# Optimization experiments

Hardware: AMD Instinct MI355X
Metric: run time of the kernel (lower is better)

The kernel has to match this reference:

```python
import jax, jax.numpy as jnp
import numpy as np

B, I, H, O = 16384, 512, 1024, 512

def setup_inputs() -> dict:
    key = jax.random.key(0)
    ks = jax.random.split(key, 8)
    s_x = 1.0 / np.sqrt(I)
    s_h = 1.0 / np.sqrt(H)
    inp = jax.random.normal(ks[0], (B, I), jnp.float32)
    h = jax.random.normal(ks[1], (B, H), jnp.float32)
    c = jax.random.normal(ks[2], (B, H), jnp.float32)
    # stacked gate weights, order [i, o, f, z]
    Wx = jax.random.uniform(ks[3], (4, H, I), jnp.float32, -s_x, s_x)
    Wh = jax.random.uniform(ks[4], (4, H, H), jnp.float32, -s_h, s_h)
    # z-gate h2z weight is re-initialized with standard normal in reset_parameters
    Wh = Wh.at[3].set(jax.random.normal(ks[5], (H, H), jnp.float32))
    # biases per module init: i=linspace(-1,-10), o=0, f=linspace(1,10), z=0
    bx = jnp.stack([
        jnp.linspace(-1.0, -10.0, H, dtype=jnp.float32),
        jnp.zeros((H,), jnp.float32),
        jnp.linspace(1.0, 10.0, H, dtype=jnp.float32),
        jnp.zeros((H,), jnp.float32),
    ])
    Wout = jax.random.uniform(ks[6], (O, H), jnp.float32, -s_h, s_h)
    bout = jax.random.uniform(ks[7], (O,), jnp.float32, -s_h, s_h)
    return {"inp": inp, "h": h, "c": c, "Wx": Wx, "bx": bx, "Wh": Wh,
            "Wout": Wout, "bout": bout}

def reference(inp, h, c, Wx, bx, Wh, Wout, bout):
    # fused gate pre-activations: two stacked GEMMs
    # gx: [4, B, H], gh: [4, B, H]
    gx = jnp.einsum('bi,ghi->gbh', inp, Wx) + bx[:, None, :]
    gh = jnp.einsum('bh,gkh->gbk', h, Wh)
    g = gx + gh
    i = jax.nn.sigmoid(g[0])
    o = jax.nn.sigmoid(g[1])
    f = jax.nn.sigmoid(g[2])
    z = jnp.tanh(g[3])
    c_new = i * z + f * c
    h_new = o * jnp.tanh(c_new)  # act_fn = tanh
    out = h_new @ Wout.T + bout
    return (out, h_new)
```

## Files before the change

kernel.cpp:

```cpp
#include <hip/hip_runtime.h>
#include <stdint.h>

#define BB 16384
#define II 512
#define HH 1024
#define OO 512

typedef short s16x8 __attribute__((ext_vector_type(8)));
typedef float f32x4 __attribute__((ext_vector_type(4)));

__device__ __forceinline__ unsigned short f2bf(float x) {
  union { float f; unsigned u; } v; v.f = x;
  return (unsigned short)((v.u + 0x7fffu + ((v.u >> 16) & 1u)) >> 16);
}
__device__ __forceinline__ float bf2f(unsigned short b) {
  union { unsigned u; float f; } v; v.u = ((unsigned)b) << 16;
  return v.f;
}
__device__ __forceinline__ float sigmoid_f(float x) {
  return 1.0f / (1.0f + __expf(-x));
}
__device__ __forceinline__ float tanh_f(float x) {
  float ax = fabsf(x);
  float e = __expf(-2.0f * ax);
  float t = (1.0f - e) / (1.0f + e);
  return x >= 0.0f ? t : -t;
}

__device__ __forceinline__ void stage16(const void* g, void* l) {
  __builtin_amdgcn_global_load_lds((const __attribute__((address_space(1))) void*)g,
                                   (__attribute__((address_space(3))) void*)l,
                                   16, 0, 0);
}

__device__ __forceinline__ void mma_step64(const unsigned short* As, const unsigned short* Bs,
                                           f32x4 acc[4][4], int lane, int wave) {
  const int wm = wave & 1, wn = wave >> 1;
  const int ln = lane & 15, q = lane >> 4;
#pragma unroll
  for (int s = 0; s < 2; ++s) {
    s16x8 af[4], bfr[4];
#pragma unroll
    for (int i = 0; i < 4; ++i) {
      const int r = wm * 64 + i * 16 + ln;
      af[i] = *(const s16x8*)(As + r * 64 + ((((s << 2) + q) + r) & 7) * 8);
    }
#pragma unroll
    for (int i = 0; i < 4; ++i) {
      const int r = wn * 64 + i * 16 + ln;
      bfr[i] = *(const s16x8*)(Bs + r * 64 + ((((s << 2) + q) + r) & 7) * 8);
    }
#pragma unroll
    for (int mi = 0; mi < 4; ++mi)
#pragma unroll
      for (int ni = 0; ni < 4; ++ni)
        acc[mi][ni] = __builtin_amdgcn_mfma_f32_16x16x32_bf16(af[mi], bfr[ni], acc[mi][ni], 0, 0, 0);
  }
}


__global__ __launch_bounds__(256) void prep_X(const float* __restrict__ inp,
                                              const float* __restrict__ h,
                                              unsigned short* __restrict__ Xb,
                                              unsigned short* __restrict__ Hlo) {
  int t = blockIdx.x * 256 + threadIdx.x;
  int base = t * 8;
  int b = base / 1536;
  int k = base - b * 1536;
  const float* src = (k < 512) ? (inp + b * 512 + k) : (h + b * 1024 + (k - 512));
  float4 v0 = *(const float4*)src;
  float4 v1 = *(const float4*)(src + 4);
  float f[8] = {v0.x, v0.y, v0.z, v0.w, v1.x, v1.y, v1.z, v1.w};
  unsigned short hi[8];
#pragma unroll
  for (int i = 0; i < 8; ++i) hi[i] = f2bf(f[i]);
  *(s16x8*)(Xb + base) = *(s16x8*)hi;
  if (k >= 512) {
    unsigned short lo[8];
#pragma unroll
    for (int i = 0; i < 8; ++i) lo[i] = f2bf(f[i] - bf2f(hi[i]));
    *(s16x8*)(Hlo + b * 1024 + (k - 512)) = *(s16x8*)lo;
  }
}

__global__ __launch_bounds__(256) void prep_Wg(const float* __restrict__ Wx,
                                               const float* __restrict__ Wh,
                                               unsigned short* __restrict__ Wg) {
  int t = blockIdx.x * 256 + threadIdx.x;
  int base = t * 8;
  int n = base / 1536;
  int k = base - n * 1536;
  int r = n & 255;
  int gate = (r >> 4) & 3;
  int unit = ((n >> 8) << 6) + (((r >> 6) & 3) << 4) + (r & 15);
  const float* src = (k < 512) ? (Wx + (gate * 1024 + unit) * 512 + k)
                               : (Wh + (gate * 1024 + unit) * 1024 + (k - 512));
  float4 v0 = *(const float4*)src;
  float4 v1 = *(const float4*)(src + 4);
  float f[8] = {v0.x, v0.y, v0.z, v0.w, v1.x, v1.y, v1.z, v1.w};
  unsigned short o[8];
#pragma unroll
  for (int i = 0; i < 8; ++i) o[i] = f2bf(f[i]);
  *(s16x8*)(Wg + base) = *(s16x8*)o;
}

__global__ __launch_bounds__(256) void prep_Wz2(const float* __restrict__ Whz,
                                                unsigned short* __restrict__ Wz2) {
  int t = blockIdx.x * 256 + threadIdx.x;
  int base = t * 8;
  int n = base >> 11;
  int k = base & 2047;
  int klo = (k < 1024) ? k : (k - 1024);
  const float* src = Whz + n * 1024 + klo;
  float4 v0 = *(const float4*)src;
  float4 v1 = *(const float4*)(src + 4);
  float f[8] = {v0.x, v0.y, v0.z, v0.w, v1.x, v1.y, v1.z, v1.w};
  unsigned short o[8];
  if (k < 1024) {
#pragma unroll
    for (int i = 0; i < 8; ++i) { unsigned short h_ = f2bf(f[i]); o[i] = f2bf(f[i] - bf2f(h_)); }
  } else {
#pragma unroll
    for (int i = 0; i < 8; ++i) o[i] = f2bf(f[i]);
  }
  *(s16x8*)(Wz2 + base) = *(s16x8*)o;
}

__global__ __launch_bounds__(256) void prep_Wout(const float* __restrict__ Wout,
                                                 unsigned short* __restrict__ Wo) {
  int t = blockIdx.x * 256 + threadIdx.x;
  int base = t * 8;
  float4 v0 = *(const float4*)(Wout + base);
  float4 v1 = *(const float4*)(Wout + base + 4);
  float f[8] = {v0.x, v0.y, v0.z, v0.w, v1.x, v1.y, v1.z, v1.w};
  unsigned short o[8];
#pragma unroll
  for (int i = 0; i < 8; ++i) o[i] = f2bf(f[i]);
  *(s16x8*)(Wo + base) = *(s16x8*)o;
}


#define RD_A(CA, MI, KS) (*(const s16x8*)((CA) + ((KS) ? aoff1 : aoff0) + (MI) * 1024))
#define RD_B(CB, NI, KS) (*(const s16x8*)((CB) + ((KS) ? boff1 : boff0) + (NI) * 1024))
#define VM4 asm volatile("s_waitcnt vmcnt(4)" ::: "memory")
#define VM0 asm volatile("s_waitcnt vmcnt(0)" ::: "memory")
#define VMNONE ((void)0)
#define NOST ((void)0)

#define ST_A(TT, HHX, DB) do { \
  stage16(gA[HHX][0] + (TT) * 64, (DB) + (HHX) * 8192); \
  stage16(gA[HHX][1] + (TT) * 64, (DB) + (HHX) * 8192 + 4096); } while (0)
#define ST_B(TT, HHX, DB) do { \
  stage16(gB[HHX][0] + (TT) * 64, (DB) + (HHX) * 8192); \
  stage16(gB[HHX][1] + (TT) * 64, (DB) + (HHX) * 8192 + 4096); } while (0)
#define ZST_A(TT, HHX, DB) do { \
  const unsigned short* g0_; const unsigned short* g1_; \
  if ((TT) < 16) { g0_ = gAX[HHX][0] + (TT) * 64; g1_ = gAX[HHX][1] + (TT) * 64; } \
  else           { g0_ = gAH[HHX][0] + ((TT) - 16) * 64; g1_ = gAH[HHX][1] + ((TT) - 16) * 64; } \
  stage16(g0_, (DB) + (HHX) * 8192); \
  stage16(g1_, (DB) + (HHX) * 8192 + 4096); } while (0)

#define PH_MFMA(Q, A00, A01, A10, A11) do { \
  __builtin_amdgcn_s_barrier(); \
  asm volatile("s_waitcnt lgkmcnt(0)" ::: "memory"); \
  __builtin_amdgcn_s_setprio(1); \
  _Pragma("unroll") \
  for (int ni = 0; ni < 4; ++ni) { \
    acc[2 * (Q)    ][ni] = __builtin_amdgcn_mfma_f32_16x16x32_bf16(A00, bq0[ni], acc[2 * (Q)    ][ni], 0, 0, 0); \
    acc[2 * (Q) + 1][ni] = __builtin_amdgcn_mfma_f32_16x16x32_bf16(A01, bq0[ni], acc[2 * (Q) + 1][ni], 0, 0, 0); \
  } \
  _Pragma("unroll") \
  for (int ni = 0; ni < 4; ++ni) { \
    acc[2 * (Q)    ][ni] = __builtin_amdgcn_mfma_f32_16x16x32_bf16(A10, bq1[ni], acc[2 * (Q)    ][ni], 0, 0, 0); \
    acc[2 * (Q) + 1][ni] = __builtin_amdgcn_mfma_f32_16x16x32_bf16(A11, bq1[ni], acc[2 * (Q) + 1][ni], 0, 0, 0); \
  } \
  __builtin_amdgcn_s_setprio(0); \
} while (0)

#define KTILE(CA, CB, S0, S1, S2, S3, VMX) do { \
  s16x8 bq0[4], bq1[4]; \
  _Pragma("unroll") \
  for (int ni = 0; ni < 4; ++ni) { bq0[ni] = RD_B(CB, ni, 0); bq1[ni] = RD_B(CB, ni, 1); } \
  s16x8 a00 = RD_A(CA, 0, 0), a01 = RD_A(CA, 1, 0); \
  s16x8 a10 = RD_A(CA, 0, 1), a11 = RD_A(CA, 1, 1); \
  S0; \
  PH_MFMA(0, a00, a01, a10, a11); \
  __builtin_amdgcn_s_barrier(); \
  a00 = RD_A(CA, 2, 0); a01 = RD_A(CA, 3, 0); a10 = RD_A(CA, 2, 1); a11 = RD_A(CA, 3, 1); \
  S1; \
  PH_MFMA(1, a00, a01, a10, a11); \
  __builtin_amdgcn_s_barrier(); \
  a00 = RD_A(CA, 4, 0); a01 = RD_A(CA, 5, 0); a10 = RD_A(CA, 4, 1); a11 = RD_A(CA, 5, 1); \
  S2; \
  PH_MFMA(2, a00, a01, a10, a11); \
  __builtin_amdgcn_s_barrier(); \
  a00 = RD_A(CA, 6, 0); a01 = RD_A(CA, 7, 0); a10 = RD_A(CA, 6, 1); a11 = RD_A(CA, 7, 1); \
  S3; \
  PH_MFMA(3, a00, a01, a10, a11); \
  VMX; \
  __builtin_amdgcn_s_barrier(); \
} while (0)

__global__ __launch_bounds__(512, 2) void gemm_gates2(const unsigned short* __restrict__ Xb,
                                                      const unsigned short* __restrict__ Wg,
                                                      const float* __restrict__ bx,
                                                      const float* __restrict__ cold,
                                                      const unsigned short* __restrict__ Dgz,
                                                      float* __restrict__ hnew,
                                                      unsigned short* __restrict__ hnewb) {
  __shared__ unsigned short lds[2][2][16384];
  const int tid = threadIdx.x;
  const int lane = tid & 63, wave = tid >> 6;
  const int wm = wave & 1, wn = wave >> 1;
  const int ln = lane & 15, qlane = lane >> 4;
  const int n0 = blockIdx.x << 8, m0 = blockIdx.y << 8;
  const int sr = tid >> 3;
  const int j = ((tid & 7) - (sr & 7)) & 7;

  const unsigned short* gA[2][2];
  const unsigned short* gB[2][2];
#pragma unroll
  for (int hh = 0; hh < 2; ++hh)
#pragma unroll
    for (int u = 0; u < 2; ++u) {
      const int row = hh * 128 + u * 64 + sr;
      gA[hh][u] = Xb + (size_t)(m0 + row) * 1536 + j * 8;
      gB[hh][u] = Wg + (size_t)(n0 + row) * 1536 + j * 8;
    }
  unsigned short* const dA0 = &lds[0][0][0] + (tid & ~63) * 8;
  unsigned short* const dB0 = &lds[0][1][0] + (tid & ~63) * 8;
  unsigned short* const dA1 = &lds[1][0][0] + (tid & ~63) * 8;
  unsigned short* const dB1 = &lds[1][1][0] + (tid & ~63) * 8;
  const unsigned short* const lA0 = &lds[0][0][0];
  const unsigned short* const lB0 = &lds[0][1][0];
  const unsigned short* const lA1 = &lds[1][0][0];
  const unsigned short* const lB1 = &lds[1][1][0];
  const int sl0 = ((qlane + ln) & 7) * 8;
  const int sl1 = sl0 ^ 32;
  const int aoff0 = (wm * 128 + ln) * 64 + sl0;
  const int aoff1 = (wm * 128 + ln) * 64 + sl1;
  const int boff0 = (wn * 64 + ln) * 64 + sl0;
  const int boff1 = (wn * 64 + ln) * 64 + sl1;

  f32x4 acc[8][4] = {};

  ST_A(0, 0, dA0); ST_A(0, 1, dA0);
  ST_B(0, 0, dB0); ST_B(0, 1, dB0);
  ST_B(1, 0, dB1); ST_B(1, 1, dB1);
  VM4;
  __builtin_amdgcn_s_barrier();

#pragma unroll 1
  for (int t = 0; t < 22; t += 2) {
    KTILE(lA0, lB0, ST_A(t + 1, 0, dA1), ST_A(t + 1, 1, dA1),
                    ST_B(t + 2, 0, dB0), ST_B(t + 2, 1, dB0), VM4);
    KTILE(lA1, lB1, ST_A(t + 2, 0, dA0), ST_A(t + 2, 1, dA0),
                    ST_B(t + 3, 0, dB1), ST_B(t + 3, 1, dB1), VM4);
  }
  KTILE(lA0, lB0, ST_A(23, 0, dA1), ST_A(23, 1, dA1), NOST, NOST, VM0);
  KTILE(lA1, lB1, NOST, NOST, NOST, NOST, VMNONE);

  const int unit = (blockIdx.x << 6) + (wn << 4) + ln;
  const float bi = bx[unit];
  const float bo = bx[1024 + unit];
  const float bfg = bx[2048 + unit];
  const float bz = bx[3072 + unit];
#pragma unroll
  for (int mi = 0; mi < 8; ++mi) {
#pragma unroll
    for (int r = 0; r < 4; ++r) {
      const int b = m0 + wm * 128 + mi * 16 + qlane * 4 + r;
      const int idx = b * 1024 + unit;
      const float gi = acc[mi][0][r] + bi;
      const float go = acc[mi][1][r] + bo;
      const float gf = acc[mi][2][r] + bfg;
      const float gz = acc[mi][3][r] + bz + bf2f(Dgz[idx]);
      const float iv = sigmoid_f(gi);
      const float ov = sigmoid_f(go);
      const float fv = sigmoid_f(gf);
      const float zv = tanh_f(gz);
      const float cn = iv * zv + fv * cold[idx];
      const float hn = ov * tanh_f(cn);
      hnew[idx] = hn;
      hnewb[idx] = f2bf(hn);
    }
  }
}

__global__ __launch_bounds__(512, 2) void gemm_zcorr2(const unsigned short* __restrict__ Xb,
                                                      const unsigned short* __restrict__ Hlo,
                                                      const unsigned short* __restrict__ Wz2,
                                                      unsigned short* __restrict__ Dgz) {
  __shared__ unsigned short lds[2][2][16384];
  const int tid = threadIdx.x;
  const int lane = tid & 63, wave = tid >> 6;
  const int wm = wave & 1, wn = wave >> 1;
  const int ln = lane & 15, qlane = lane >> 4;
  const int n0 = blockIdx.x << 8, m0 = blockIdx.y << 8;
  const int sr = tid >> 3;
  const int j = ((tid & 7) - (sr & 7)) & 7;

  const unsigned short* gAX[2][2];
  const unsigned short* gAH[2][2];
  const unsigned short* gB[2][2];
#pragma unroll
  for (int hh = 0; hh < 2; ++hh)
#pragma unroll
    for (int u = 0; u < 2; ++u) {
      const int row = hh * 128 + u * 64 + sr;
      gAX[hh][u] = Xb  + (size_t)(m0 + row) * 1536 + 512 + j * 8;
      gAH[hh][u] = Hlo + (size_t)(m0 + row) * 1024 + j * 8;
      gB[hh][u]  = Wz2 + (size_t)(n0 + row) * 2048 + j * 8;
    }
  unsigned short* const dA0 = &lds[0][0][0] + (tid & ~63) * 8;
  unsigned short* const dB0 = &lds[0][1][0] + (tid & ~63) * 8;
  unsigned short* const dA1 = &lds[1][0][0] + (tid & ~63) * 8;
  unsigned short* const dB1 = &lds[1][1][0] + (tid & ~63) * 8;
  const unsigned short* const lA0 = &lds[0][0][0];
  const unsigned short* const lB0 = &lds[0][1][0];
  const unsigned short* const lA1 = &lds[1][0][0];
  const unsigned short* const lB1 = &lds[1][1][0];
  const int sl0 = ((qlane + ln) & 7) * 8;
  const int sl1 = sl0 ^ 32;
  const int aoff0 = (wm * 128 + ln) * 64 + sl0;
  const int aoff1 = (wm * 128 + ln) * 64 + sl1;
  const int boff0 = (wn * 64 + ln) * 64 + sl0;
  const int boff1 = (wn * 64 + ln) * 64 + sl1;

  f32x4 acc[8][4] = {};

  ZST_A(0, 0, dA0); ZST_A(0, 1, dA0);
  ST_B(0, 0, dB0);  ST_B(0, 1, dB0);
  ST_B(1, 0, dB1);  ST_B(1, 1, dB1);
  VM4;
  __builtin_amdgcn_s_barrier();

#pragma unroll 1
  for (int t = 0; t < 30; t += 2) {
    KTILE(lA0, lB0, ZST_A(t + 1, 0, dA1), ZST_A(t + 1, 1, dA1),
                    ST_B(t + 2, 0, dB0),  ST_B(t + 2, 1, dB0), VM4);
    KTILE(lA1, lB1, ZST_A(t + 2, 0, dA0), ZST_A(t + 2, 1, dA0),
                    ST_B(t + 3, 0, dB1),  ST_B(t + 3, 1, dB1), VM4);
  }
  KTILE(lA0, lB0, ZST_A(31, 0, dA1), ZST_A(31, 1, dA1), NOST, NOST, VM0);
  KTILE(lA1, lB1, NOST, NOST, NOST, NOST, VMNONE);

#pragma unroll
  for (int mi = 0; mi < 8; ++mi) {
#pragma unroll
    for (int r = 0; r < 4; ++r) {
      const int b = m0 + wm * 128 + mi * 16 + qlane * 4 + r;
#pragma unroll
      for (int ni = 0; ni < 4; ++ni) {
        const int n = n0 + wn * 64 + ni * 16 + ln;
        Dgz[b * 1024 + n] = f2bf(acc[mi][ni][r]);
      }
    }
  }
}

__global__ __launch_bounds__(256) void gemm_out(const unsigned short* __restrict__ Hb,
                                                const unsigned short* __restrict__ Wo,
                                                const float* __restrict__ bout,
                                                float* __restrict__ out) {
  __shared__ unsigned short As[8192];
  __shared__ unsigned short Bs[8192];
  const int n0 = blockIdx.x * 128;
  const int m0 = blockIdx.y * 128;
  const int tid = threadIdx.x, lane = tid & 63, wave = tid >> 6;
  const unsigned short *ga[4], *gb[4];
  unsigned short *la[4], *lb[4];
#pragma unroll
  for (int u = 0; u < 4; ++u) {
    int p = u * 256 + tid;
    int r = p >> 3;
    int jj = ((p & 7) - r) & 7;
    ga[u] = Hb + (size_t)(m0 + r) * 1024 + jj * 8;
    gb[u] = Wo + (size_t)(n0 + r) * 1024 + jj * 8;
    la[u] = As + (u * 256 + (tid & ~63)) * 8;
    lb[u] = Bs + (u * 256 + (tid & ~63)) * 8;
  }
  f32x4 acc[4][4] = {};
  for (int kk = 0; kk < 16; ++kk) {
#pragma unroll
    for (int u = 0; u < 4; ++u) { stage16(ga[u], la[u]); stage16(gb[u], lb[u]); }
#pragma unroll
    for (int u = 0; u < 4; ++u) { ga[u] += 64; gb[u] += 64; }
    __syncthreads();
    mma_step64(As, Bs, acc, lane, wave);
    __syncthreads();
  }
  const int wm = wave & 1, wn = wave >> 1;
  const int ln = lane & 15, q = lane >> 4;
  float bo_[4];
#pragma unroll
  for (int ni = 0; ni < 4; ++ni) bo_[ni] = bout[n0 + wn * 64 + ni * 16 + ln];
#pragma unroll
  for (int mi = 0; mi < 4; ++mi) {
#pragma unroll
    for (int r = 0; r < 4; ++r) {
      const int b = m0 + wm * 64 + mi * 16 + q * 4 + r;
#pragma unroll
      for (int ni = 0; ni < 4; ++ni) {
        const int n = n0 + wn * 64 + ni * 16 + ln;
        out[b * 512 + n] = acc[mi][ni][r] + bo_[ni];
      }
    }
  }
}

extern "C" void kernel_launch(void* const* d_in, const int* in_sizes, int n_in,
                              void* d_out, int out_size, void* d_ws, size_t ws_size,
                              hipStream_t stream) {
  const float* inp  = (const float*)d_in[0];
  const float* h    = (const float*)d_in[1];
  const float* c    = (const float*)d_in[2];
  const float* Wx   = (const float*)d_in[3];
  const float* bx   = (const float*)d_in[4];
  const float* Wh   = (const float*)d_in[5];
  const float* Wout = (const float*)d_in[6];
  const float* bout = (const float*)d_in[7];

  float* out  = (float*)d_out;
  float* hnew = out + (size_t)BB * OO;

  char* ws = (char*)d_ws;
  unsigned short* Xb  = (unsigned short*)(ws);
  unsigned short* Wg  = (unsigned short*)(ws + 50331648);
  unsigned short* Wo  = (unsigned short*)(ws + 62914560);
  unsigned short* Hb  = (unsigned short*)(ws + 63963136);
  unsigned short* Hlo = (unsigned short*)(ws + 97517568);
  unsigned short* Wz2 = (unsigned short*)(ws + 131072000);
  unsigned short* Dgz = (unsigned short*)(ws + 135266304);

  prep_X   <<<12288, 256, 0, stream>>>(inp, h, Xb, Hlo);
  prep_Wg  <<<3072,  256, 0, stream>>>(Wx, Wh, Wg);
  prep_Wz2 <<<1024,  256, 0, stream>>>(Wh + 3 * 1024 * 1024, Wz2);
  prep_Wout<<<256,   256, 0, stream>>>(Wout, Wo);
  gemm_zcorr2<<<dim3(4, 64),  512, 0, stream>>>(Xb, Hlo, Wz2, Dgz);
  gemm_gates2<<<dim3(16, 64), 512, 0, stream>>>(Xb, Wg, bx, c, Dgz, hnew, Hb);
  gemm_out  <<<dim3(4, 128),  256, 0, stream>>>(Hb, Wo, bout, out);
}
```

Measured before the change: 556.2 us.

## Restructure GEMM k-tile pipeline and swizzle block order across XCDs

Reworks the double-buffered GEMM main loop so whole A and B tiles are staged for tile t+2 into the buffer just consumed, with A fragments read in two batched groups of four, a vmcnt(8) wait and sched_barriers around the MFMA phases. It also remaps block indices in all three GEMM kernels so consecutive workgroups, assumed to be spread round-robin over the 8 XCDs, land on neighbouring tiles and share L2 reuse. The goal is fewer stalls on LDS and global loads and better cache locality. In exchange it holds more A-fragment registers, which could lower occupancy or cause spills, and the ordering of buffer reuse against the barriers must stay correct.

```diff
diff --git a/kernel.cpp b/kernel.cpp
--- a/kernel.cpp
+++ b/kernel.cpp
@@ -142,27 +142,39 @@
 
 #define RD_A(CA, MI, KS) (*(const s16x8*)((CA) + ((KS) ? aoff1 : aoff0) + (MI) * 1024))
 #define RD_B(CB, NI, KS) (*(const s16x8*)((CB) + ((KS) ? boff1 : boff0) + (NI) * 1024))
-#define VM4 asm volatile("s_waitcnt vmcnt(4)" ::: "memory")
+#define VM8 asm volatile("s_waitcnt vmcnt(8)" ::: "memory")
 #define VM0 asm volatile("s_waitcnt vmcnt(0)" ::: "memory")
+#define LGKM0 asm volatile("s_waitcnt lgkmcnt(0)" ::: "memory")
 #define VMNONE ((void)0)
 #define NOST ((void)0)
 
-#define ST_A(TT, HHX, DB) do { \
-  stage16(gA[HHX][0] + (TT) * 64, (DB) + (HHX) * 8192); \
-  stage16(gA[HHX][1] + (TT) * 64, (DB) + (HHX) * 8192 + 4096); } while (0)
-#define ST_B(TT, HHX, DB) do { \
-  stage16(gB[HHX][0] + (TT) * 64, (DB) + (HHX) * 8192); \
-  stage16(gB[HHX][1] + (TT) * 64, (DB) + (HHX) * 8192 + 4096); } while (0)
-#define ZST_A(TT, HHX, DB) do { \
-  const unsigned short* g0_; const unsigned short* g1_; \
-  if ((TT) < 16) { g0_ = gAX[HHX][0] + (TT) * 64; g1_ = gAX[HHX][1] + (TT) * 64; } \
-  else           { g0_ = gAH[HHX][0] + ((TT) - 16) * 64; g1_ = gAH[HHX][1] + ((TT) - 16) * 64; } \
-  stage16(g0_, (DB) + (HHX) * 8192); \
-  stage16(g1_, (DB) + (HHX) * 8192 + 4096); } while (0)
-
-#define PH_MFMA(Q, A00, A01, A10, A11) do { \
+#define ST_A2(TT, DB) do { \
+  stage16(gA[0][0] + (size_t)(TT) * 64, (DB)); \
+  stage16(gA[0][1] + (size_t)(TT) * 64, (DB) + 4096); \
+  stage16(gA[1][0] + (size_t)(TT) * 64, (DB) + 8192); \
+  stage16(gA[1][1] + (size_t)(TT) * 64, (DB) + 12288); } while (0)
+#define ST_B2(TT, DB) do { \
+  stage16(gB[0][0] + (size_t)(TT) * 64, (DB)); \
+  stage16(gB[0][1] + (size_t)(TT) * 64, (DB) + 4096); \
+  stage16(gB[1][0] + (size_t)(TT) * 64, (DB) + 8192); \
+  stage16(gB[1][1] + (size_t)(TT) * 64, (DB) + 12288); } while (0)
+#define ZST_A2(TT, DB) do { \
+  const unsigned short *z0_, *z1_, *z2_, *z3_; \
+  if ((TT) < 16) { \
+    z0_ = gAX[0][0] + (size_t)(TT) * 64; z1_ = gAX[0][1] + (size_t)(TT) * 64; \
+    z2_ = gAX[1][0] + (size_t)(TT) * 64; z3_ = gAX[1][1] + (size_t)(TT) * 64; \
+  } else { \
+    const int tz_ = (TT) - 16; \
+    z0_ = gAH[0][0] + (size_t)tz_ * 64; z1_ = gAH[0][1] + (size_t)tz_ * 64; \
+    z2_ = gAH[1][0] + (size_t)tz_ * 64; z3_ = gAH[1][1] + (size_t)tz_ * 64; \
+  } \
+  stage16(z0_, (DB)); stage16(z1_, (DB) + 4096); \
+  stage16(z2_, (DB) + 8192); stage16(z3_, (DB) + 12288); } while (0)
+
+#define PH(Q, WAIT, A00, A01, A10, A11) do { \
   __builtin_amdgcn_s_barrier(); \
-  asm volatile("s_waitcnt lgkmcnt(0)" ::: "memory"); \
+  WAIT; \
+  __builtin_amdgcn_sched_barrier(0); \
   __builtin_amdgcn_s_setprio(1); \
   _Pragma("unroll") \
   for (int ni = 0; ni < 4; ++ni) { \
@@ -177,26 +189,24 @@
   __builtin_amdgcn_s_setprio(0); \
 } while (0)
 
-#define KTILE(CA, CB, S0, S1, S2, S3, VMX) do { \
-  s16x8 bq0[4], bq1[4]; \
+#define KTILE2(CA, CB, SB2, SA2, VMX) do { \
+  s16x8 bq0[4], bq1[4], p0[4], p1[4]; \
   _Pragma("unroll") \
   for (int ni = 0; ni < 4; ++ni) { bq0[ni] = RD_B(CB, ni, 0); bq1[ni] = RD_B(CB, ni, 1); } \
-  s16x8 a00 = RD_A(CA, 0, 0), a01 = RD_A(CA, 1, 0); \
-  s16x8 a10 = RD_A(CA, 0, 1), a11 = RD_A(CA, 1, 1); \
-  S0; \
-  PH_MFMA(0, a00, a01, a10, a11); \
+  _Pragma("unroll") \
+  for (int mi = 0; mi < 4; ++mi) { p0[mi] = RD_A(CA, mi, 0); p1[mi] = RD_A(CA, mi, 1); } \
+  PH(0, LGKM0, p0[0], p0[1], p1[0], p1[1]); \
   __builtin_amdgcn_s_barrier(); \
-  a00 = RD_A(CA, 2, 0); a01 = RD_A(CA, 3, 0); a10 = RD_A(CA, 2, 1); a11 = RD_A(CA, 3, 1); \
-  S1; \
-  PH_MFMA(1, a00, a01, a10, a11); \
+  s16x8 r0[4], r1[4]; \
+  _Pragma("unroll") \
+  for (int mi = 0; mi < 4; ++mi) { r0[mi] = RD_A(CA, 4 + mi, 0); r1[mi] = RD_A(CA, 4 + mi, 1); } \
+  SB2; \
+  PH(1, VMNONE, p0[2], p0[3], p1[2], p1[3]); \
   __builtin_amdgcn_s_barrier(); \
-  a00 = RD_A(CA, 4, 0); a01 = RD_A(CA, 5, 0); a10 = RD_A(CA, 4, 1); a11 = RD_A(CA, 5, 1); \
-  S2; \
-  PH_MFMA(2, a00, a01, a10, a11); \
+  PH(2, LGKM0, r0[0], r0[1], r1[0], r1[1]); \
   __builtin_amdgcn_s_barrier(); \
-  a00 = RD_A(CA, 6, 0); a01 = RD_A(CA, 7, 0); a10 = RD_A(CA, 6, 1); a11 = RD_A(CA, 7, 1); \
-  S3; \
-  PH_MFMA(3, a00, a01, a10, a11); \
+  SA2; \
+  PH(3, VMNONE, r0[2], r0[3], r1[2], r1[3]); \
   VMX; \
   __builtin_amdgcn_s_barrier(); \
 } while (0)
@@ -213,7 +223,10 @@
   const int lane = tid & 63, wave = tid >> 6;
   const int wm = wave & 1, wn = wave >> 1;
   const int ln = lane & 15, qlane = lane >> 4;
-  const int n0 = blockIdx.x << 8, m0 = blockIdx.y << 8;
+  const int fid = (int)(blockIdx.y * 16 + blockIdx.x);
+  const int swz = ((fid & 7) << 7) + (fid >> 3);
+  const int bxi = swz & 15, byi = swz >> 4;
+  const int n0 = bxi << 8, m0 = byi << 8;
   const int sr = tid >> 3;
   const int j = ((tid & 7) - (sr & 7)) & 7;
 
@@ -244,23 +257,20 @@
 
   f32x4 acc[8][4] = {};
 
-  ST_A(0, 0, dA0); ST_A(0, 1, dA0);
-  ST_B(0, 0, dB0); ST_B(0, 1, dB0);
-  ST_B(1, 0, dB1); ST_B(1, 1, dB1);
-  VM4;
+  ST_A2(0, dA0); ST_B2(0, dB0);
+  ST_A2(1, dA1); ST_B2(1, dB1);
+  VM8;
   __builtin_amdgcn_s_barrier();
 
 #pragma unroll 1
   for (int t = 0; t < 22; t += 2) {
-    KTILE(lA0, lB0, ST_A(t + 1, 0, dA1), ST_A(t + 1, 1, dA1),
-                    ST_B(t + 2, 0, dB0), ST_B(t + 2, 1, dB0), VM4);
-    KTILE(lA1, lB1, ST_A(t + 2, 0, dA0), ST_A(t + 2, 1, dA0),
-                    ST_B(t + 3, 0, dB1), ST_B(t + 3, 1, dB1), VM4);
-  }
-  KTILE(lA0, lB0, ST_A(23, 0, dA1), ST_A(23, 1, dA1), NOST, NOST, VM0);
-  KTILE(lA1, lB1, NOST, NOST, NOST, NOST, VMNONE);
-
-  const int unit = (blockIdx.x << 6) + (wn << 4) + ln;
+    KTILE2(lA0, lB0, ST_B2(t + 2, dB0), ST_A2(t + 2, dA0), VM8);
+    KTILE2(lA1, lB1, ST_B2(t + 3, dB1), ST_A2(t + 3, dA1), VM8);
+  }
+  KTILE2(lA0, lB0, NOST, NOST, VM0);
+  KTILE2(lA1, lB1, NOST, NOST, VMNONE);
+
+  const int unit = (bxi << 6) + (wn << 4) + ln;
   const float bi = bx[unit];
   const float bo = bx[1024 + unit];
   const float bfg = bx[2048 + unit];
@@ -296,7 +306,10 @@
   const int lane = tid & 63, wave = tid >> 6;
   const int wm = wave & 1, wn = wave >> 1;
   const int ln = lane & 15, qlane = lane >> 4;
-  const int n0 = blockIdx.x << 8, m0 = blockIdx.y << 8;
+  const int fid = (int)(blockIdx.y * 4 + blockIdx.x);
+  const int swz = ((fid & 7) << 5) + (fid >> 3);
+  const int bxi = swz & 3, byi = swz >> 2;
+  const int n0 = bxi << 8, m0 = byi << 8;
   const int sr = tid >> 3;
   const int j = ((tid & 7) - (sr & 7)) & 7;
 
@@ -329,21 +342,18 @@
 
   f32x4 acc[8][4] = {};
 
-  ZST_A(0, 0, dA0); ZST_A(0, 1, dA0);
-  ST_B(0, 0, dB0);  ST_B(0, 1, dB0);
-  ST_B(1, 0, dB1);  ST_B(1, 1, dB1);
-  VM4;
+  ZST_A2(0, dA0); ST_B2(0, dB0);
+  ZST_A2(1, dA1); ST_B2(1, dB1);
+  VM8;
   __builtin_amdgcn_s_barrier();
 
 #pragma unroll 1
   for (int t = 0; t < 30; t += 2) {
-    KTILE(lA0, lB0, ZST_A(t + 1, 0, dA1), ZST_A(t + 1, 1, dA1),
-                    ST_B(t + 2, 0, dB0),  ST_B(t + 2, 1, dB0), VM4);
-    KTILE(lA1, lB1, ZST_A(t + 2, 0, dA0), ZST_A(t + 2, 1, dA0),
-                    ST_B(t + 3, 0, dB1),  ST_B(t + 3, 1, dB1), VM4);
-  }
-  KTILE(lA0, lB0, ZST_A(31, 0, dA1), ZST_A(31, 1, dA1), NOST, NOST, VM0);
-  KTILE(lA1, lB1, NOST, NOST, NOST, NOST, VMNONE);
+    KTILE2(lA0, lB0, ST_B2(t + 2, dB0), ZST_A2(t + 2, dA0), VM8);
+    KTILE2(lA1, lB1, ST_B2(t + 3, dB1), ZST_A2(t + 3, dA1), VM8);
+  }
+  KTILE2(lA0, lB0, NOST, NOST, VM0);
+  KTILE2(lA1, lB1, NOST, NOST, VMNONE);
 
 #pragma unroll
   for (int mi = 0; mi < 8; ++mi) {
@@ -365,8 +375,10 @@
                                                 float* __restrict__ out) {
   __shared__ unsigned short As[8192];
   __shared__ unsigned short Bs[8192];
-  const int n0 = blockIdx.x * 128;
-  const int m0 = blockIdx.y * 128;
+  const int fid = (int)(blockIdx.y * 4 + blockIdx.x);
+  const int swz = ((fid & 7) << 6) + (fid >> 3);
+  const int n0 = (swz & 3) * 128;
+  const int m0 = (swz >> 2) * 128;
   const int tid = threadIdx.x, lane = tid & 63, wave = tid >> 6;
   const unsigned short *ga[4], *gb[4];
   unsigned short *la[4], *lb[4];
```

Measured after the change: 590.4 us. +6.1%, slower.
